# Kernel optimization log

Hardware: AMD Instinct MI355X
Metric: run time of the kernel (lower is better)

The kernel has to match this reference:

```python
import jax, jax.numpy as jnp
import numpy as np

N_NODES = 100000
N_EDGES = 3200000
NFEAT = 256
NHID = 256


def setup_inputs() -> dict:
    key = jax.random.key(0)
    ks = jax.random.split(key, 8)
    x = jax.random.normal(ks[0], (N_NODES, NFEAT), dtype=jnp.float32)
    # Glorot-ish scaled weights
    W1 = jax.random.normal(ks[1], (NFEAT, NHID), dtype=jnp.float32) / np.sqrt(NFEAT)
    b1 = jax.random.normal(ks[2], (NHID,), dtype=jnp.float32) * 0.01
    W2 = jax.random.normal(ks[3], (NHID, NHID), dtype=jnp.float32) / np.sqrt(NHID)
    b2 = jax.random.normal(ks[4], (NHID,), dtype=jnp.float32) * 0.01
    edge_weight = jax.random.uniform(ks[5], (N_EDGES,), dtype=jnp.float32)
    edge_src = jax.random.randint(ks[6], (N_EDGES,), 0, N_NODES, dtype=jnp.int32)
    edge_dst = jax.random.randint(ks[7], (N_EDGES,), 0, N_NODES, dtype=jnp.int32)
    return {
        "x": x, "W1": W1, "b1": b1, "W2": W2, "b2": b2,
        "edge_weight": edge_weight, "edge_src": edge_src, "edge_dst": edge_dst,
    }


def _gcn_layer(x, W, b, edge_weight, edge_src, edge_dst):
    # support = x @ W  (dense GEMM, [N, d_out])
    support = x @ W
    # spmm(adj, support): gather source rows, scale by edge weight, scatter-add to dst
    msgs = support[edge_src] * edge_weight[:, None]          # [E, d_out]
    agg = jax.ops.segment_sum(msgs, edge_dst, num_segments=N_NODES)
    return agg + b


def reference(x, W1, b1, W2, b2, edge_weight, edge_src, edge_dst):
    # Eval mode: F.dropout is identity (training=False).
    h = jax.nn.elu(_gcn_layer(x, W1, b1, edge_weight, edge_src, edge_dst))
    h = jax.nn.elu(_gcn_layer(h, W2, b2, edge_weight, edge_src, edge_dst))
    return h
```

## Files before the change

kernel.cpp:

```cpp
#include <hip/hip_runtime.h>
#include <math.h>

#define N_NODES 100000
#define N_EDGES 3200000
#define NF 256

typedef unsigned short u16;
typedef unsigned int u32;

typedef __bf16 bf16x8_t __attribute__((ext_vector_type(8)));
typedef float f32x4_t __attribute__((ext_vector_type(4)));

union U8 { uint4 q; u16 s[8]; };

typedef __attribute__((address_space(1))) const void* as1_cvp;
typedef __attribute__((address_space(3))) void* as3_vp;

__device__ __forceinline__ float bf2f(u16 u) {
  union { u32 i; float f; } v; v.i = ((u32)u) << 16; return v.f;
}
__device__ __forceinline__ u16 f2bf(float f) {
  union { float f; u32 i; } v; v.f = f;
  u32 x = v.i;
  u32 r = (x + 0x7FFFu + ((x >> 16) & 1u)) >> 16;
  return (u16)r;
}
__device__ __forceinline__ float u2f(u32 u) {
  union { u32 i; float f; } v; v.i = u; return v.f;
}

__device__ __forceinline__ void gload_lds16(const u16* g, u16* l) {
  __builtin_amdgcn_global_load_lds((as1_cvp)g, (as3_vp)l, 16, 0, 0);
}

__global__ void sniff_kernel(const u16* __restrict__ xr, int* __restrict__ flag) {
  __shared__ int cnt;
  if (threadIdx.x == 0) cnt = 0;
  __syncthreads();
  int c = 0;
  for (int i = threadIdx.x; i < 65536; i += 256) {
    u16 u = xr[i];
    if ((u & 0x7F80u) == 0x7F80u) c++;
  }
  atomicAdd(&cnt, c);
  __syncthreads();
  if (threadIdx.x == 0) flag[0] = (cnt >= 4) ? 1 : 0;
}

__global__ void prep_all(const int* __restrict__ dst, int* __restrict__ counts,
                         int* __restrict__ rank,
                         const float* __restrict__ xf, u16* __restrict__ xbf,
                         const u16* __restrict__ W1u, const float* __restrict__ W1f,
                         const u16* __restrict__ W2u, const float* __restrict__ W2f,
                         const u16* __restrict__ b1u, const float* __restrict__ b1f,
                         const u16* __restrict__ b2u, const float* __restrict__ b2f,
                         const int* __restrict__ flagp,
                         u16* __restrict__ Wt1, u16* __restrict__ Wt2,
                         u16* __restrict__ bb1, u16* __restrict__ bb2) {
  int b = blockIdx.x;
  int t = threadIdx.x;
  if (b < 12500) {
    int e = b * 256 + t;
    rank[e] = atomicAdd(&counts[dst[e]], 1);
  } else if (b < 25000) {
    if (!flagp[0]) return;
    size_t i = ((size_t)(b - 12500) * 256 + t) * 8;
    float4 a = *(const float4*)(xf + i);
    float4 c = *(const float4*)(xf + i + 4);
    U8 o;
    o.s[0] = f2bf(a.x); o.s[1] = f2bf(a.y); o.s[2] = f2bf(a.z); o.s[3] = f2bf(a.w);
    o.s[4] = f2bf(c.x); o.s[5] = f2bf(c.y); o.s[6] = f2bf(c.z); o.s[7] = f2bf(c.w);
    *(uint4*)(xbf + i) = o.q;
  } else {
    int pb = b - 25000;
    int isf = flagp[0];
    if (pb < 256) {
      Wt1[t * NF + pb] = isf ? f2bf(W1f[pb * NF + t]) : W1u[pb * NF + t];
    } else if (pb < 512) {
      int k = pb - 256;
      Wt2[t * NF + k] = isf ? f2bf(W2f[k * NF + t]) : W2u[k * NF + t];
    } else if (pb == 512) {
      bb1[t] = isf ? f2bf(b1f[t]) : b1u[t];
    } else {
      bb2[t] = isf ? f2bf(b2f[t]) : b2u[t];
    }
  }
}

__global__ void scanA(const int* __restrict__ counts, int* __restrict__ partial) {
  __shared__ int s[256];
  int t = threadIdx.x;
  int gid = blockIdx.x * 256 + t;
  int v = (gid < N_NODES) ? counts[gid] : 0;
  s[t] = v;
  __syncthreads();
  for (int offd = 128; offd > 0; offd >>= 1) {
    if (t < offd) s[t] += s[t + offd];
    __syncthreads();
  }
  if (t == 0) partial[blockIdx.x] = s[0];
}

__global__ void scanB(int* __restrict__ partial) {
  const int NPART = 391;
  __shared__ int s[512];
  int t = threadIdx.x;
  int v = (t < NPART) ? partial[t] : 0;
  s[t] = v;
  __syncthreads();
  for (int offd = 1; offd < 512; offd <<= 1) {
    int x = 0;
    if (t >= offd) x = s[t - offd];
    __syncthreads();
    s[t] += x;
    __syncthreads();
  }
  if (t < NPART) partial[t] = (t == 0) ? 0 : s[t - 1];
}

__global__ void scanC(const int* __restrict__ counts, const int* __restrict__ partial,
                      int* __restrict__ offs) {
  __shared__ int s[256];
  int t = threadIdx.x;
  int b = blockIdx.x;
  int gid = b * 256 + t;
  int v = (gid < N_NODES) ? counts[gid] : 0;
  s[t] = v;
  __syncthreads();
  for (int offd = 1; offd < 256; offd <<= 1) {
    int x = 0;
    if (t >= offd) x = s[t - offd];
    __syncthreads();
    s[t] += x;
    __syncthreads();
  }
  int incl = s[t];
  if (gid < N_NODES) offs[gid] = partial[b] + (incl - v);
  if (gid == N_NODES - 1) offs[N_NODES] = partial[b] + incl;
}

__global__ void place_pack(const int* __restrict__ src, const int* __restrict__ dst,
                           const u16* __restrict__ wu, const float* __restrict__ wf,
                           const int* __restrict__ flagp, const int* __restrict__ offs,
                           const int* __restrict__ rank, uint2* __restrict__ rec) {
  int e = blockIdx.x * 256 + threadIdx.x;
  int pos = offs[dst[e]] + rank[e];
  float w = flagp[0] ? wf[e] : bf2f(wu[e]);
  uint2 r;
  r.x = (u32)src[e];
  r.y = __float_as_uint(w);
  rec[pos] = r;
}

__global__ void place_full(const int* __restrict__ src, const int* __restrict__ dst,
                           const u16* __restrict__ wu, const float* __restrict__ wf,
                           const int* __restrict__ flagp, const int* __restrict__ offs,
                           const int* __restrict__ rank,
                           int* __restrict__ ssrc, u16* __restrict__ sw) {
  int e = blockIdx.x * 256 + threadIdx.x;
  int pos = offs[dst[e]] + rank[e];
  ssrc[pos] = src[e];
  if (flagp[0]) sw[pos] = f2bf(wf[e]);
  else          sw[pos] = wu[e];
}

__global__ void place_eid(const int* __restrict__ dst, const int* __restrict__ offs,
                          const int* __restrict__ rank, int* __restrict__ seid) {
  int e = blockIdx.x * 256 + threadIdx.x;
  seid[offs[dst[e]] + rank[e]] = e;
}

__global__ __launch_bounds__(256) void gemm_gll(
    const u16* __restrict__ A0, const u16* __restrict__ A1,
    const u16* __restrict__ Bt, u16* __restrict__ C, int M,
    const int* __restrict__ flagp) {
  __shared__ __align__(16) u16 Al[2][128 * 32];
  __shared__ __align__(16) u16 Bl[2][128 * 32];
  const u16* A = flagp[0] ? A1 : A0;
  const int tid = threadIdx.x;
  const int m0 = blockIdx.x * 128;
  const int n0 = blockIdx.y * 128;
  const int lane = tid & 63;
  const int wave = tid >> 6;
  const int wm = (wave & 1) * 64;
  const int wn = (wave >> 1) * 64;
  const int mrow = lane & 15;
  const int grp = lane >> 4;

  f32x4_t acc[4][4];
  const f32x4_t zero = {0.f, 0.f, 0.f, 0.f};
#pragma unroll
  for (int i = 0; i < 4; ++i)
#pragma unroll
    for (int j = 0; j < 4; ++j) acc[i][j] = zero;

  const int rA = lane >> 2;
  const int cA = (lane & 3) * 8;
  const int r0 = wave * 32;

  auto stage = [&](int buf, int k0) {
#pragma unroll
    for (int c = 0; c < 2; ++c) {
      int rr = r0 + c * 16;
      int ar = rr + rA;
      int gm = m0 + ar;
      if (gm >= M) gm = 0;
      gload_lds16(A + (size_t)gm * NF + k0 + cA, &Al[buf][rr * 32]);
      gload_lds16(Bt + (size_t)(n0 + ar) * NF + k0 + cA, &Bl[buf][rr * 32]);
    }
  };

  stage(0, 0);
  __syncthreads();

  for (int t = 0; t < 8; ++t) {
    int cur = t & 1;
    if (t < 7) stage(cur ^ 1, (t + 1) * 32);
    bf16x8_t af[4], bfr[4];
#pragma unroll
    for (int i = 0; i < 4; ++i)
      af[i] = *(const bf16x8_t*)(&Al[cur][(wm + i * 16 + mrow) * 32 + grp * 8]);
#pragma unroll
    for (int j = 0; j < 4; ++j)
      bfr[j] = *(const bf16x8_t*)(&Bl[cur][(wn + j * 16 + mrow) * 32 + grp * 8]);
#pragma unroll
    for (int i = 0; i < 4; ++i)
#pragma unroll
      for (int j = 0; j < 4; ++j)
        acc[i][j] = __builtin_amdgcn_mfma_f32_16x16x32_bf16(bfr[j], af[i], acc[i][j], 0, 0, 0);
    __syncthreads();
  }

#pragma unroll
  for (int i = 0; i < 4; ++i) {
    int row = m0 + wm + i * 16 + mrow;
    if (row >= M) continue;
#pragma unroll
    for (int j = 0; j < 4; ++j) {
      u16 pk[4];
      pk[0] = f2bf(acc[i][j][0]);
      pk[1] = f2bf(acc[i][j][1]);
      pk[2] = f2bf(acc[i][j][2]);
      pk[3] = f2bf(acc[i][j][3]);
      *(uint2*)(C + (size_t)row * NF + n0 + wn + j * 16 + grp * 4) = *(const uint2*)pk;
    }
  }
}

__global__ __launch_bounds__(256) void agg_pack(
    const u16* __restrict__ sup, const int* __restrict__ offs,
    const uint2* __restrict__ rec,
    const u16* __restrict__ bbf, u16* __restrict__ out2, float* __restrict__ out4,
    const int* __restrict__ flagp, int outmask) {
  int node = blockIdx.x * 4 + (threadIdx.x >> 6);
  int lane = threadIdx.x & 63;
  int half = lane >> 5;
  int c0 = (lane & 31) * 8;
  float a0 = 0.f, a1 = 0.f, a2 = 0.f, a3 = 0.f, a4 = 0.f, a5 = 0.f, a6 = 0.f, a7 = 0.f;
  int eend = offs[node + 1];
  int e = offs[node] + half;

  for (; e + 6 < eend; e += 8) {
    uint2 r0 = rec[e], r1 = rec[e + 2], r2 = rec[e + 4], r3 = rec[e + 6];
    float w0 = u2f(r0.y), w1 = u2f(r1.y), w2 = u2f(r2.y), w3 = u2f(r3.y);
    U8 v0, v1, v2, v3;
    v0.q = *(const uint4*)(sup + (((u32)r0.x) << 8) + c0);
    v1.q = *(const uint4*)(sup + (((u32)r1.x) << 8) + c0);
    v2.q = *(const uint4*)(sup + (((u32)r2.x) << 8) + c0);
    v3.q = *(const uint4*)(sup + (((u32)r3.x) << 8) + c0);
    a0 += bf2f(v0.s[0]) * w0; a1 += bf2f(v0.s[1]) * w0; a2 += bf2f(v0.s[2]) * w0; a3 += bf2f(v0.s[3]) * w0;
    a4 += bf2f(v0.s[4]) * w0; a5 += bf2f(v0.s[5]) * w0; a6 += bf2f(v0.s[6]) * w0; a7 += bf2f(v0.s[7]) * w0;
    a0 += bf2f(v1.s[0]) * w1; a1 += bf2f(v1.s[1]) * w1; a2 += bf2f(v1.s[2]) * w1; a3 += bf2f(v1.s[3]) * w1;
    a4 += bf2f(v1.s[4]) * w1; a5 += bf2f(v1.s[5]) * w1; a6 += bf2f(v1.s[6]) * w1; a7 += bf2f(v1.s[7]) * w1;
    a0 += bf2f(v2.s[0]) * w2; a1 += bf2f(v2.s[1]) * w2; a2 += bf2f(v2.s[2]) * w2; a3 += bf2f(v2.s[3]) * w2;
    a4 += bf2f(v2.s[4]) * w2; a5 += bf2f(v2.s[5]) * w2; a6 += bf2f(v2.s[6]) * w2; a7 += bf2f(v2.s[7]) * w2;
    a0 += bf2f(v3.s[0]) * w3; a1 += bf2f(v3.s[1]) * w3; a2 += bf2f(v3.s[2]) * w3; a3 += bf2f(v3.s[3]) * w3;
    a4 += bf2f(v3.s[4]) * w3; a5 += bf2f(v3.s[5]) * w3; a6 += bf2f(v3.s[6]) * w3; a7 += bf2f(v3.s[7]) * w3;
  }
  for (; e < eend; e += 2) {
    uint2 r0 = rec[e];
    float w0 = u2f(r0.y);
    U8 v0;
    v0.q = *(const uint4*)(sup + (((u32)r0.x) << 8) + c0);
    a0 += bf2f(v0.s[0]) * w0; a1 += bf2f(v0.s[1]) * w0; a2 += bf2f(v0.s[2]) * w0; a3 += bf2f(v0.s[3]) * w0;
    a4 += bf2f(v0.s[4]) * w0; a5 += bf2f(v0.s[5]) * w0; a6 += bf2f(v0.s[6]) * w0; a7 += bf2f(v0.s[7]) * w0;
  }

  a0 += __shfl_xor(a0, 32); a1 += __shfl_xor(a1, 32);
  a2 += __shfl_xor(a2, 32); a3 += __shfl_xor(a3, 32);
  a4 += __shfl_xor(a4, 32); a5 += __shfl_xor(a5, 32);
  a6 += __shfl_xor(a6, 32); a7 += __shfl_xor(a7, 32);

  if (half == 0) {
    U8 bv; bv.q = *(const uint4*)(bbf + c0);
    float r0 = a0 + bf2f(bv.s[0]);
    float r1 = a1 + bf2f(bv.s[1]);
    float r2 = a2 + bf2f(bv.s[2]);
    float r3 = a3 + bf2f(bv.s[3]);
    float r4 = a4 + bf2f(bv.s[4]);
    float r5 = a5 + bf2f(bv.s[5]);
    float r6 = a6 + bf2f(bv.s[6]);
    float r7 = a7 + bf2f(bv.s[7]);
    r0 = r0 > 0.f ? r0 : expm1f(r0);
    r1 = r1 > 0.f ? r1 : expm1f(r1);
    r2 = r2 > 0.f ? r2 : expm1f(r2);
    r3 = r3 > 0.f ? r3 : expm1f(r3);
    r4 = r4 > 0.f ? r4 : expm1f(r4);
    r5 = r5 > 0.f ? r5 : expm1f(r5);
    r6 = r6 > 0.f ? r6 : expm1f(r6);
    r7 = r7 > 0.f ? r7 : expm1f(r7);
    if (outmask && flagp[0]) {
      float4 o4a, o4b;
      o4a.x = r0; o4a.y = r1; o4a.z = r2; o4a.w = r3;
      o4b.x = r4; o4b.y = r5; o4b.z = r6; o4b.w = r7;
      *(float4*)(out4 + (size_t)node * NF + c0) = o4a;
      *(float4*)(out4 + (size_t)node * NF + c0 + 4) = o4b;
    } else {
      U8 o;
      o.s[0] = f2bf(r0); o.s[1] = f2bf(r1); o.s[2] = f2bf(r2); o.s[3] = f2bf(r3);
      o.s[4] = f2bf(r4); o.s[5] = f2bf(r5); o.s[6] = f2bf(r6); o.s[7] = f2bf(r7);
      *(uint4*)(out2 + (size_t)node * NF + c0) = o.q;
    }
  }
}

__global__ __launch_bounds__(256) void agg_full(
    const u16* __restrict__ sup, const int* __restrict__ offs,
    const int* __restrict__ ssrc, const u16* __restrict__ sw,
    const u16* __restrict__ bbf, u16* __restrict__ out2, float* __restrict__ out4,
    const int* __restrict__ flagp, int outmask) {
  int node = blockIdx.x * 4 + (threadIdx.x >> 6);
  int lane = threadIdx.x & 63;
  int half = lane >> 5;
  int c0 = (lane & 31) * 8;
  float a0 = 0.f, a1 = 0.f, a2 = 0.f, a3 = 0.f, a4 = 0.f, a5 = 0.f, a6 = 0.f, a7 = 0.f;
  int eend = offs[node + 1];
  int e = offs[node] + half;

  for (; e + 6 < eend; e += 8) {
    int s0 = ssrc[e], s1 = ssrc[e + 2], s2 = ssrc[e + 4], s3 = ssrc[e + 6];
    float w0 = bf2f(sw[e]), w1 = bf2f(sw[e + 2]), w2 = bf2f(sw[e + 4]), w3 = bf2f(sw[e + 6]);
    U8 v0, v1, v2, v3;
    v0.q = *(const uint4*)(sup + (((u32)s0) << 8) + c0);
    v1.q = *(const uint4*)(sup + (((u32)s1) << 8) + c0);
    v2.q = *(const uint4*)(sup + (((u32)s2) << 8) + c0);
    v3.q = *(const uint4*)(sup + (((u32)s3) << 8) + c0);
    a0 += bf2f(v0.s[0]) * w0; a1 += bf2f(v0.s[1]) * w0; a2 += bf2f(v0.s[2]) * w0; a3 += bf2f(v0.s[3]) * w0;
    a4 += bf2f(v0.s[4]) * w0; a5 += bf2f(v0.s[5]) * w0; a6 += bf2f(v0.s[6]) * w0; a7 += bf2f(v0.s[7]) * w0;
    a0 += bf2f(v1.s[0]) * w1; a1 += bf2f(v1.s[1]) * w1; a2 += bf2f(v1.s[2]) * w1; a3 += bf2f(v1.s[3]) * w1;
    a4 += bf2f(v1.s[4]) * w1; a5 += bf2f(v1.s[5]) * w1; a6 += bf2f(v1.s[6]) * w1; a7 += bf2f(v1.s[7]) * w1;
    a0 += bf2f(v2.s[0]) * w2; a1 += bf2f(v2.s[1]) * w2; a2 += bf2f(v2.s[2]) * w2; a3 += bf2f(v2.s[3]) * w2;
    a4 += bf2f(v2.s[4]) * w2; a5 += bf2f(v2.s[5]) * w2; a6 += bf2f(v2.s[6]) * w2; a7 += bf2f(v2.s[7]) * w2;
    a0 += bf2f(v3.s[0]) * w3; a1 += bf2f(v3.s[1]) * w3; a2 += bf2f(v3.s[2]) * w3; a3 += bf2f(v3.s[3]) * w3;
    a4 += bf2f(v3.s[4]) * w3; a5 += bf2f(v3.s[5]) * w3; a6 += bf2f(v3.s[6]) * w3; a7 += bf2f(v3.s[7]) * w3;
  }
  for (; e < eend; e += 2) {
    int s0 = ssrc[e];
    float w0 = bf2f(sw[e]);
    U8 v0;
    v0.q = *(const uint4*)(sup + (((u32)s0) << 8) + c0);
    a0 += bf2f(v0.s[0]) * w0; a1 += bf2f(v0.s[1]) * w0; a2 += bf2f(v0.s[2]) * w0; a3 += bf2f(v0.s[3]) * w0;
    a4 += bf2f(v0.s[4]) * w0; a5 += bf2f(v0.s[5]) * w0; a6 += bf2f(v0.s[6]) * w0; a7 += bf2f(v0.s[7]) * w0;
  }

  a0 += __shfl_xor(a0, 32); a1 += __shfl_xor(a1, 32);
  a2 += __shfl_xor(a2, 32); a3 += __shfl_xor(a3, 32);
  a4 += __shfl_xor(a4, 32); a5 += __shfl_xor(a5, 32);
  a6 += __shfl_xor(a6, 32); a7 += __shfl_xor(a7, 32);

  if (half == 0) {
    U8 bv; bv.q = *(const uint4*)(bbf + c0);
    float r0 = a0 + bf2f(bv.s[0]);
    float r1 = a1 + bf2f(bv.s[1]);
    float r2 = a2 + bf2f(bv.s[2]);
    float r3 = a3 + bf2f(bv.s[3]);
    float r4 = a4 + bf2f(bv.s[4]);
    float r5 = a5 + bf2f(bv.s[5]);
    float r6 = a6 + bf2f(bv.s[6]);
    float r7 = a7 + bf2f(bv.s[7]);
    r0 = r0 > 0.f ? r0 : expm1f(r0);
    r1 = r1 > 0.f ? r1 : expm1f(r1);
    r2 = r2 > 0.f ? r2 : expm1f(r2);
    r3 = r3 > 0.f ? r3 : expm1f(r3);
    r4 = r4 > 0.f ? r4 : expm1f(r4);
    r5 = r5 > 0.f ? r5 : expm1f(r5);
    r6 = r6 > 0.f ? r6 : expm1f(r6);
    r7 = r7 > 0.f ? r7 : expm1f(r7);
    if (outmask && flagp[0]) {
      float4 o4a, o4b;
      o4a.x = r0; o4a.y = r1; o4a.z = r2; o4a.w = r3;
      o4b.x = r4; o4b.y = r5; o4b.z = r6; o4b.w = r7;
      *(float4*)(out4 + (size_t)node * NF + c0) = o4a;
      *(float4*)(out4 + (size_t)node * NF + c0 + 4) = o4b;
    } else {
      U8 o;
      o.s[0] = f2bf(r0); o.s[1] = f2bf(r1); o.s[2] = f2bf(r2); o.s[3] = f2bf(r3);
      o.s[4] = f2bf(r4); o.s[5] = f2bf(r5); o.s[6] = f2bf(r6); o.s[7] = f2bf(r7);
      *(uint4*)(out2 + (size_t)node * NF + c0) = o.q;
    }
  }
}

__global__ __launch_bounds__(256) void agg_eid(
    const u16* __restrict__ sup, const int* __restrict__ offs,
    const int* __restrict__ seid, const int* __restrict__ esrc,
    const u16* __restrict__ ewu, const float* __restrict__ ewf,
    const u16* __restrict__ bbf, u16* __restrict__ out2, float* __restrict__ out4,
    const int* __restrict__ flagp, int outmask) {
  int node = blockIdx.x * 4 + (threadIdx.x >> 6);
  int lane = threadIdx.x & 63;
  int c0 = lane * 4;
  int isf = flagp[0];
  float a0 = 0.f, a1 = 0.f, a2 = 0.f, a3 = 0.f;
  int e = offs[node];
  int eend = offs[node + 1];
  for (; e < eend; ++e) {
    int eid = seid[e];
    int src = esrc[eid];
    float w = isf ? ewf[eid] : bf2f(ewu[eid]);
    ushort4 v = *(const ushort4*)(sup + (size_t)src * NF + c0);
    a0 += bf2f(v.x) * w;
    a1 += bf2f(v.y) * w;
    a2 += bf2f(v.z) * w;
    a3 += bf2f(v.w) * w;
  }
  ushort4 bv = *(const ushort4*)(bbf + c0);
  float r0 = a0 + bf2f(bv.x);
  float r1 = a1 + bf2f(bv.y);
  float r2 = a2 + bf2f(bv.z);
  float r3 = a3 + bf2f(bv.w);
  r0 = r0 > 0.f ? r0 : expm1f(r0);
  r1 = r1 > 0.f ? r1 : expm1f(r1);
  r2 = r2 > 0.f ? r2 : expm1f(r2);
  r3 = r3 > 0.f ? r3 : expm1f(r3);
  if (outmask && isf) {
    float4 o4;
    o4.x = r0; o4.y = r1; o4.z = r2; o4.w = r3;
    *(float4*)(out4 + (size_t)node * NF + c0) = o4;
  } else {
    ushort4 o;
    o.x = f2bf(r0); o.y = f2bf(r1); o.z = f2bf(r2); o.w = f2bf(r3);
    *(ushort4*)(out2 + (size_t)node * NF + c0) = o;
  }
}

extern "C" void kernel_launch(void* const* d_in, const int* in_sizes, int n_in,
                              void* d_out, int out_size, void* d_ws, size_t ws_size,
                              hipStream_t stream) {
  const u16* x2    = (const u16*)d_in[0];
  const float* x4  = (const float*)d_in[0];
  const u16* W1u   = (const u16*)d_in[1];
  const float* W1f = (const float*)d_in[1];
  const u16* b1u   = (const u16*)d_in[2];
  const float* b1f = (const float*)d_in[2];
  const u16* W2u   = (const u16*)d_in[3];
  const float* W2f = (const float*)d_in[3];
  const u16* b2u   = (const u16*)d_in[4];
  const float* b2f = (const float*)d_in[4];
  const u16* ewu   = (const u16*)d_in[5];
  const float* ewf = (const float*)d_in[5];
  const int* esrc  = (const int*)d_in[6];
  const int* edst  = (const int*)d_in[7];
  u16* out2  = (u16*)d_out;
  float* out4 = (float*)d_out;

  char* ws = (char*)d_ws;
  size_t oWt1     = 0;
  size_t oWt2     = 131072;
  size_t oSup     = 262144;
  size_t oCounts  = 51462144;
  size_t oOffs    = 51862528;
  size_t oPartial = 52663296;
  size_t oFlag    = 52665344;
  size_t oBb1     = 52665600;
  size_t oBb2     = 52666624;
  size_t oTail    = 52667648;
  size_t need_pack  = oTail + (size_t)N_EDGES * 8;
  size_t need_split = oTail + 12800000 + 6400000;

  u16* Wt1     = (u16*)(ws + oWt1);
  u16* Wt2     = (u16*)(ws + oWt2);
  u16* sup     = (u16*)(ws + oSup);
  int* rank    = (int*)(ws + oSup);
  int* counts  = (int*)(ws + oCounts);
  int* offs    = (int*)(ws + oOffs);
  int* partial = (int*)(ws + oPartial);
  int* flag    = (int*)(ws + oFlag);
  u16* bb1     = (u16*)(ws + oBb1);
  u16* bb2     = (u16*)(ws + oBb2);

  u16* h1  = out2;
  u16* xbf = (u16*)((char*)d_out + (size_t)N_NODES * NF * 2);

  sniff_kernel<<<1, 256, 0, stream>>>(x2, flag);
  hipMemsetAsync(counts, 0, (size_t)N_NODES * 4, stream);
  prep_all<<<25514, 256, 0, stream>>>(edst, counts, rank, x4, xbf,
                                      W1u, W1f, W2u, W2f, b1u, b1f, b2u, b2f,
                                      flag, Wt1, Wt2, bb1, bb2);
  scanA<<<391, 256, 0, stream>>>(counts, partial);
  scanB<<<1, 512, 0, stream>>>(partial);
  scanC<<<391, 256, 0, stream>>>(counts, partial, offs);

  dim3 ggrid((N_NODES + 127) / 128, 2);

  if (ws_size >= need_pack) {
    uint2* rec = (uint2*)(ws + oTail);
    place_pack<<<N_EDGES / 256, 256, 0, stream>>>(esrc, edst, ewu, ewf, flag, offs, rank, rec);
    gemm_gll<<<ggrid, 256, 0, stream>>>(x2, xbf, Wt1, sup, N_NODES, flag);
    agg_pack<<<N_NODES / 4, 256, 0, stream>>>(sup, offs, rec, bb1, h1, out4, flag, 0);
    gemm_gll<<<ggrid, 256, 0, stream>>>(h1, h1, Wt2, sup, N_NODES, flag);
    agg_pack<<<N_NODES / 4, 256, 0, stream>>>(sup, offs, rec, bb2, out2, out4, flag, 1);
  } else if (ws_size >= need_split) {
    int* ssrc = (int*)(ws + oTail);
    u16* sw   = (u16*)(ws + oTail + 12800000);
    place_full<<<N_EDGES / 256, 256, 0, stream>>>(esrc, edst, ewu, ewf, flag, offs, rank, ssrc, sw);
    gemm_gll<<<ggrid, 256, 0, stream>>>(x2, xbf, Wt1, sup, N_NODES, flag);
    agg_full<<<N_NODES / 4, 256, 0, stream>>>(sup, offs, ssrc, sw, bb1, h1, out4, flag, 0);
    gemm_gll<<<ggrid, 256, 0, stream>>>(h1, h1, Wt2, sup, N_NODES, flag);
    agg_full<<<N_NODES / 4, 256, 0, stream>>>(sup, offs, ssrc, sw, bb2, out2, out4, flag, 1);
  } else {
    int* seid = (int*)(ws + oTail);
    place_eid<<<N_EDGES / 256, 256, 0, stream>>>(edst, offs, rank, seid);
    gemm_gll<<<ggrid, 256, 0, stream>>>(x2, xbf, Wt1, sup, N_NODES, flag);
    agg_eid<<<N_NODES / 4, 256, 0, stream>>>(sup, offs, seid, esrc, ewu, ewf, bb1, h1, out4, flag, 0);
    gemm_gll<<<ggrid, 256, 0, stream>>>(h1, h1, Wt2, sup, N_NODES, flag);
    agg_eid<<<N_NODES / 4, 256, 0, stream>>>(sup, offs, seid, esrc, ewu, ewf, bb2, out2, out4, flag, 1);
  }
}
```

Measured before the change: 971.3 us.

## Fuse first GEMM with edge placement kernel via interleaved block roles

Merges the edge-record placement pass and the first dense GEMM into one launch. Every ninth block runs a GEMM tile and the rest scatter packed (src, weight) records. This lets the memory-bound scatter overlap with the compute-bound GEMM instead of running them serially. Rank now lives in a separate tail buffer rather than aliasing the support buffer, which needs more workspace. The old path is kept as a fallback when the workspace is too small, and the pack branch is removed from it.

```diff
diff --git a/kernel.cpp b/kernel.cpp
--- a/kernel.cpp
+++ b/kernel.cpp
@@ -139,17 +139,104 @@
   if (gid == N_NODES - 1) offs[N_NODES] = partial[b] + incl;
 }
 
-__global__ void place_pack(const int* __restrict__ src, const int* __restrict__ dst,
-                           const u16* __restrict__ wu, const float* __restrict__ wf,
-                           const int* __restrict__ flagp, const int* __restrict__ offs,
-                           const int* __restrict__ rank, uint2* __restrict__ rec) {
-  int e = blockIdx.x * 256 + threadIdx.x;
-  int pos = offs[dst[e]] + rank[e];
-  float w = flagp[0] ? wf[e] : bf2f(wu[e]);
-  uint2 r;
-  r.x = (u32)src[e];
-  r.y = __float_as_uint(w);
-  rec[pos] = r;
+#define GEMM_CNT 1564
+#define FUSE_GRID 14068
+
+__global__ __launch_bounds__(256) void gemm1_place(
+    const u16* __restrict__ A0, const u16* __restrict__ A1,
+    const u16* __restrict__ Bt, u16* __restrict__ C, int M,
+    const int* __restrict__ flagp,
+    const int* __restrict__ src, const int* __restrict__ dst,
+    const u16* __restrict__ wu, const float* __restrict__ wf,
+    const int* __restrict__ offs, const int* __restrict__ rank,
+    uint2* __restrict__ rec) {
+  __shared__ __align__(16) u16 Al[2][128 * 32];
+  __shared__ __align__(16) u16 Bl[2][128 * 32];
+  const int bx = blockIdx.x;
+  const int tid = threadIdx.x;
+
+  if (bx % 9 != 0) {
+    int pidx = bx - (bx / 9 + 1);
+    if (pidx >= 12500) return;
+    int e = pidx * 256 + tid;
+    int pos = offs[dst[e]] + rank[e];
+    float w = flagp[0] ? wf[e] : bf2f(wu[e]);
+    uint2 r;
+    r.x = (u32)src[e];
+    r.y = __float_as_uint(w);
+    rec[pos] = r;
+    return;
+  }
+
+  const int gi = bx / 9;
+  const u16* A = flagp[0] ? A1 : A0;
+  const int m0 = (gi >> 1) * 128;
+  const int n0 = (gi & 1) * 128;
+  const int lane = tid & 63;
+  const int wave = tid >> 6;
+  const int wm = (wave & 1) * 64;
+  const int wn = (wave >> 1) * 64;
+  const int mrow = lane & 15;
+  const int grp = lane >> 4;
+
+  f32x4_t acc[4][4];
+  const f32x4_t zero = {0.f, 0.f, 0.f, 0.f};
+#pragma unroll
+  for (int i = 0; i < 4; ++i)
+#pragma unroll
+    for (int j = 0; j < 4; ++j) acc[i][j] = zero;
+
+  const int rA = lane >> 2;
+  const int cA = (lane & 3) * 8;
+  const int r0 = wave * 32;
+
+  auto stage = [&](int buf, int k0) {
+#pragma unroll
+    for (int c = 0; c < 2; ++c) {
+      int rr = r0 + c * 16;
+      int ar = rr + rA;
+      int gm = m0 + ar;
+      if (gm >= M) gm = 0;
+      gload_lds16(A + (size_t)gm * NF + k0 + cA, &Al[buf][rr * 32]);
+      gload_lds16(Bt + (size_t)(n0 + ar) * NF + k0 + cA, &Bl[buf][rr * 32]);
+    }
+  };
+
+  stage(0, 0);
+  __syncthreads();
+
+  for (int t = 0; t < 8; ++t) {
+    int cur = t & 1;
+    if (t < 7) stage(cur ^ 1, (t + 1) * 32);
+    bf16x8_t af[4], bfr[4];
+#pragma unroll
+    for (int i = 0; i < 4; ++i)
+      af[i] = *(const bf16x8_t*)(&Al[cur][(wm + i * 16 + mrow) * 32 + grp * 8]);
+#pragma unroll
+    for (int j = 0; j < 4; ++j)
+      bfr[j] = *(const bf16x8_t*)(&Bl[cur][(wn + j * 16 + mrow) * 32 + grp * 8]);
+#pragma unroll
+    for (int i = 0; i < 4; ++i)
+#pragma unroll
+      for (int j = 0; j < 4; ++j)
+        acc[i][j] = __builtin_amdgcn_mfma_f32_16x16x32_bf16(bfr[j], af[i], acc[i][j], 0, 0, 0);
+    __syncthreads();
+  }
+
+#pragma unroll
+  for (int i = 0; i < 4; ++i) {
+    int row = m0 + wm + i * 16 + mrow;
+    if (row >= M) continue;
+#pragma unroll
+    for (int j = 0; j < 4; ++j) {
+      u16 pk[4];
+      pk[0] = f2bf(acc[i][j][0]);
+      pk[1] = f2bf(acc[i][j][1]);
+      pk[2] = f2bf(acc[i][j][2]);
+      pk[3] = f2bf(acc[i][j][3]);
+      *(uint2*)(C + (size_t)row * NF + n0 + wn + j * 16 + grp * 4) = *(const uint2*)pk;
+    }
+  }
 }
 
 __global__ void place_full(const int* __restrict__ src, const int* __restrict__ dst,
@@ -489,8 +576,30 @@
   u16* bb1     = (u16*)(ws + oBb1);
   u16* bb2     = (u16*)(ws + oBb2);
 
+  size_t need_fused = oTail + (size_t)N_EDGES * 8 + (size_t)N_EDGES * 4;
+
   u16* h1  = out2;
   u16* xbf = (u16*)((char*)d_out + (size_t)N_NODES * NF * 2);
+
+  if (ws_size >= need_fused) {
+    uint2* rec   = (uint2*)(ws + oTail);
+    int* rank_t  = (int*)(ws + oTail + (size_t)N_EDGES * 8);
+
+    sniff_kernel<<<1, 256, 0, stream>>>(x2, flag);
+    hipMemsetAsync(counts, 0, (size_t)N_NODES * 4, stream);
+    prep_all<<<25514, 256, 0, stream>>>(edst, counts, rank_t, x4, xbf,
+                                        W1u, W1f, W2u, W2f, b1u, b1f, b2u, b2f,
+                                        flag, Wt1, Wt2, bb1, bb2);
+    scanA<<<391, 256, 0, stream>>>(counts, partial);
+    scanB<<<1, 512, 0, stream>>>(partial);
+    scanC<<<391, 256, 0, stream>>>(counts, partial, offs);
+    gemm1_place<<<FUSE_GRID, 256, 0, stream>>>(x2, xbf, Wt1, sup, N_NODES, flag,
+                                               esrc, edst, ewu, ewf, offs, rank_t, rec);
+    agg_pack<<<N_NODES / 4, 256, 0, stream>>>(sup, offs, rec, bb1, h1, out4, flag, 0);
+    gemm_gll<<<dim3((N_NODES + 127) / 128, 2), 256, 0, stream>>>(h1, h1, Wt2, sup, N_NODES, flag);
+    agg_pack<<<N_NODES / 4, 256, 0, stream>>>(sup, offs, rec, bb2, out2, out4, flag, 1);
+    return;
+  }
 
   sniff_kernel<<<1, 256, 0, stream>>>(x2, flag);
   hipMemsetAsync(counts, 0, (size_t)N_NODES * 4, stream);
@@ -503,14 +612,7 @@
 
   dim3 ggrid((N_NODES + 127) / 128, 2);
 
-  if (ws_size >= need_pack) {
-    uint2* rec = (uint2*)(ws + oTail);
-    place_pack<<<N_EDGES / 256, 256, 0, stream>>>(esrc, edst, ewu, ewf, flag, offs, rank, rec);
-    gemm_gll<<<ggrid, 256, 0, stream>>>(x2, xbf, Wt1, sup, N_NODES, flag);
-    agg_pack<<<N_NODES / 4, 256, 0, stream>>>(sup, offs, rec, bb1, h1, out4, flag, 0);
-    gemm_gll<<<ggrid, 256, 0, stream>>>(h1, h1, Wt2, sup, N_NODES, flag);
-    agg_pack<<<N_NODES / 4, 256, 0, stream>>>(sup, offs, rec, bb2, out2, out4, flag, 1);
-  } else if (ws_size >= need_split) {
+  if (ws_size >= need_split) {
     int* ssrc = (int*)(ws + oTail);
     u16* sw   = (u16*)(ws + oTail + 12800000);
     place_full<<<N_EDGES / 256, 256, 0, stream>>>(esrc, edst, ewu, ewf, flag, offs, rank, ssrc, sw);
```

Measured after the change: 966.0 us. About the same (-0.5%).
